# Kernel tuning notes

Measured on AMD Instinct MI355X. Metric: run time of the kernel, lower is better.

Reference implementation:

```python
import jax, jax.numpy as jnp
import numpy as np

NCONST = 100
NFEATS = 16
NCLASS = 5
NEFF = 6
NDYN = 6
BN_EPS = 1e-3  # keras BatchNormalization default epsilon


def _edge_indices(nconst):
    # itertools.product order, skipping self-pairs, matching _build_relation_matrices
    recv, send = [], []
    for i in range(nconst):
        for j in range(nconst):
            if i != j:
                recv.append(i)
                send.append(j)
    return np.asarray(recv, np.int32), np.asarray(send, np.int32)


def setup_inputs() -> dict:
    key = jax.random.key(0)
    ks = jax.random.split(key, 16)

    def w(k, shape, fan_in):
        return (jax.random.normal(k, shape, jnp.float32) / np.sqrt(fan_in)).astype(jnp.float32)

    inp = {
        "x": jax.random.normal(ks[0], (512, NCONST, NFEATS), jnp.float32),
        # batchnorm (inference-mode) params over the feature axis
        "bn_gamma": jnp.ones((NFEATS,), jnp.float32),
        "bn_beta": jnp.zeros((NFEATS,), jnp.float32),
        "bn_mean": jnp.zeros((NFEATS,), jnp.float32),
        "bn_var": jnp.ones((NFEATS,), jnp.float32),
        # fr: pointwise Conv1D == dense over last dim; 2*nfeats -> 30 -> 15 -> 6
        "fr_w1": w(ks[1], (2 * NFEATS, 30), 2 * NFEATS), "fr_b1": jnp.zeros((30,), jnp.float32),
        "fr_w2": w(ks[2], (30, 15), 30), "fr_b2": jnp.zeros((15,), jnp.float32),
        "fr_w3": w(ks[3], (15, NEFF), 15), "fr_b3": jnp.zeros((NEFF,), jnp.float32),
        # fo: (nfeats + neffects) -> 45 -> 22 -> 6
        "fo_w1": w(ks[4], (NFEATS + NEFF, 45), NFEATS + NEFF), "fo_b1": jnp.zeros((45,), jnp.float32),
        "fo_w2": w(ks[5], (45, 22), 45), "fo_b2": jnp.zeros((22,), jnp.float32),
        "fo_w3": w(ks[6], (22, NDYN), 22), "fo_b3": jnp.zeros((NDYN,), jnp.float32),
        # fc: ndyn -> 48 -> nclasses (softmax)
        "fc_w1": w(ks[7], (NDYN, 48), NDYN), "fc_b1": jnp.zeros((48,), jnp.float32),
        "fc_w2": w(ks[8], (48, NCLASS), 48), "fc_b2": jnp.zeros((NCLASS,), jnp.float32),
    }
    return inp


def reference(x, bn_gamma, bn_beta, bn_mean, bn_var,
              fr_w1, fr_b1, fr_w2, fr_b2, fr_w3, fr_b3,
              fo_w1, fo_b1, fo_w2, fo_b2, fo_w3, fo_b3,
              fc_w1, fc_b1, fc_w2, fc_b2):
    nconst = x.shape[1]
    recv_idx, send_idx = _edge_indices(nconst)  # static, shape (nedges,)

    # BatchNormalization (inference) over the feature axis: (B, N, F)
    xb = (x - bn_mean) * jax.lax.rsqrt(bn_var + BN_EPS) * bn_gamma + bn_beta

    # One-hot relation matmuls are exact gathers: (B, E, F) each.
    # Concat order matches Concatenate(axis=1)([receiver, sender]) pre-permute.
    fr_in = jnp.concatenate([xb[:, recv_idx, :], xb[:, send_idx, :]], axis=-1)  # (B, E, 2F)

    h = jax.nn.relu(fr_in @ fr_w1 + fr_b1)
    h = jax.nn.relu(h @ fr_w2 + fr_b2)
    effects = jax.nn.relu(h @ fr_w3 + fr_b3)  # (B, E, neff)

    # Multiplying by receiver_matrix^T is a scatter-add of edge effects to receiver nodes.
    agg = jnp.zeros((x.shape[0], nconst, effects.shape[-1]), effects.dtype)
    agg = agg.at[:, recv_idx, :].add(effects)  # (B, N, neff)

    fo_in = jnp.concatenate([xb, agg], axis=-1)  # (B, N, F + neff)
    d = jax.nn.relu(fo_in @ fo_w1 + fo_b1)
    d = jax.nn.relu(d @ fo_w2 + fo_b2)
    d = jax.nn.relu(d @ fo_w3 + fo_b3)  # (B, N, ndyn)

    fc_in = jnp.sum(d, axis=1)  # summation=True -> (B, ndyn)
    h = jax.nn.relu(fc_in @ fc_w1 + fc_b1)
    logits = h @ fc_w2 + fc_b2
    return jax.nn.softmax(logits, axis=-1)  # (B, nclasses)
```

## Files before the change

kernel.cpp:

```cpp
#include <hip/hip_runtime.h>
#include <math.h>

#define NCONST 100
#define NF     16
#define BLK    512

typedef _Float16 f16;
typedef _Float16 f16x8 __attribute__((ext_vector_type(8)));
typedef _Float16 f16x4 __attribute__((ext_vector_type(4)));
typedef float    f32x16 __attribute__((ext_vector_type(16)));

__global__ __launch_bounds__(BLK, 4) void convint_fused(
    const float* __restrict__ x,
    const float* __restrict__ bn_g, const float* __restrict__ bn_b,
    const float* __restrict__ bn_m, const float* __restrict__ bn_v,
    const float* __restrict__ frw1, const float* __restrict__ frb1,
    const float* __restrict__ frw2, const float* __restrict__ frb2,
    const float* __restrict__ frw3, const float* __restrict__ frb3,
    const float* __restrict__ fow1, const float* __restrict__ fob1,
    const float* __restrict__ fow2, const float* __restrict__ fob2,
    const float* __restrict__ fow3, const float* __restrict__ fob3,
    const float* __restrict__ fcw1, const float* __restrict__ fcb1,
    const float* __restrict__ fcw2, const float* __restrict__ fcb2,
    float* __restrict__ out)
{
    __shared__ float xbn[NCONST][NF];
    __shared__ float upool[7200];
    __shared__ float aggF[NCONST * 8];
    __shared__ float fcin[8];
    __shared__ float hfc[48];
    __shared__ float logits[8];

    char* const PrB = (char*)upool;
    char* const PsB = PrB + 8000;
    float (*const foh1)[48] = (float (*)[48])upool;
    float (*const foh2)[24] = (float (*)[24])(upool + 4800);

    const int b   = blockIdx.x;
    const int tid = threadIdx.x;
    const float* xb = x + (size_t)b * (NCONST * NF);

    for (int idx = tid; idx < NCONST * NF; idx += BLK) {
        int f = idx & 15;
        float sc = rsqrtf(bn_v[f] + 1e-3f) * bn_g[f];
        xbn[idx >> 4][f] = (xb[idx] - bn_m[f]) * sc + bn_b[f];
    }
    if (tid < 8) fcin[tid] = 0.f;
    __syncthreads();

    for (int idx = tid; idx < 1600; idx += BLK) {
        int n   = idx >> 4;
        int rem = idx & 15;
        int sel = rem >> 3;
        int oq  = rem & 7;
        int o0  = oq * 4;
        float xs[16];
        {
            const float4* xv = (const float4*)(&xbn[n][0]);
            float4 x0 = xv[0], x1 = xv[1], x2 = xv[2], x3 = xv[3];
            xs[0]=x0.x; xs[1]=x0.y; xs[2]=x0.z; xs[3]=x0.w;
            xs[4]=x1.x; xs[5]=x1.y; xs[6]=x1.z; xs[7]=x1.w;
            xs[8]=x2.x; xs[9]=x2.y; xs[10]=x2.z; xs[11]=x2.w;
            xs[12]=x3.x; xs[13]=x3.y; xs[14]=x3.z; xs[15]=x3.w;
        }
        float acc0 = (!sel) ? frb1[o0 + 0] : 0.f;
        float acc1 = (!sel) ? frb1[o0 + 1] : 0.f;
        float acc2 = (!sel && oq < 7) ? frb1[o0 + 2] : 0.f;
        float acc3 = (!sel && oq < 7) ? frb1[o0 + 3] : 0.f;
        const float* wbase = frw1 + sel * 16 * 30;
        const int wcol2 = (oq < 7) ? o0 + 2 : 28;
        #pragma unroll
        for (int f = 0; f < 16; ++f) {
            const float* wr = wbase + f * 30;
            float2 wa = *(const float2*)(wr + o0);
            float2 wb = *(const float2*)(wr + wcol2);
            acc0 = fmaf(xs[f], wa.x, acc0);
            acc1 = fmaf(xs[f], wa.y, acc1);
            acc2 = fmaf(xs[f], wb.x, acc2);
            acc3 = fmaf(xs[f], wb.y, acc3);
        }
        f16x4 hv;
        hv[0] = (f16)acc0;
        hv[1] = (f16)acc1;
        hv[2] = (oq < 7) ? (f16)acc2 : (sel ? (f16)0.f : (f16)1.f);
        hv[3] = (oq < 7) ? (f16)acc3 : (f16)0.f;
        int slot = oq >> 1;
        int sw = (slot & 2) | ((slot ^ (n >> 3)) & 1);
        *(f16x4*)((sel ? PsB : PrB) + n * 80 + sw * 16 + (oq & 1) * 8) = hv;
    }
    __syncthreads();

    {
        const int l  = tid & 63;
        const int wv = tid >> 6;
        const int e  = l & 31;
        const int hi = l >> 5;

        const int o2p = (e >= 4 && e < 12) ? (e ^ 12) : e;
        const bool o2v = (o2p < 15);
        const int  o2c = o2v ? o2p : 0;
        const bool o3v = (e < 6);
        const int  o3c = o3v ? e : 0;

        f16x8 bf1a, bf1b, bf2p;
        #pragma unroll
        for (int m = 0; m < 8; ++m) {
            int ka  = hi * 8 + m;
            int kb_ = 16 + ka;
            bf1a[m] = o2v ? (f16)frw2[ka * 15 + o2c] : (f16)0.f;
            f16 wb = (f16)0.f;
            if (o2v) {
                if (kb_ < 30)       wb = (f16)frw2[kb_ * 15 + o2c];
                else if (kb_ == 30) wb = (f16)frb2[o2c];
            }
            bf1b[m] = wb;
            f16 w3 = (f16)0.f;
            if (o3v) {
                if (ka < 15)       w3 = (f16)frw3[ka * 6 + o3c];
                else               w3 = (f16)frb3[o3c];
            }
            bf2p[m] = w3;
        }
        f32x16 cz;
        #pragma unroll
        for (int r = 0; r < 16; ++r) cz[r] = 0.f;
        const float gtail = (e < 3) ? 1.f : 0.f;

        for (int base = wv; base < 50; base += 8) {
            const int iA = base, iB = base + 50;
            const char* prpA = PrB + iA * 80 + ((hi ^ ((iA >> 3) & 1)) * 16);
            const char* prpB = PrB + iB * 80 + ((hi ^ ((iB >> 3) & 1)) * 16);
            f16x8 praA = *(const f16x8*)prpA;
            f16x8 prbA = *(const f16x8*)(prpA + 32);
            f16x8 praB = *(const f16x8*)prpB;
            f16x8 prbB = *(const f16x8*)(prpB + 32);
            float a0 = 0.f, a1 = 0.f, a2r = 0.f, a3 = 0.f;
            float b0 = 0.f, b1 = 0.f, b2r = 0.f, b3 = 0.f;

            int jA = iA + 1 + e; if (jA >= 100) jA -= 100;
            int jB = iB + 1 + e; if (jB >= 100) jB -= 100;
            #pragma unroll
            for (int tb = 0; tb < 4; ++tb) {
                const char* pspA = PsB + jA * 80 + ((hi ^ ((jA >> 3) & 1)) * 16);
                const char* pspB = PsB + jB * 80 + ((hi ^ ((jB >> 3) & 1)) * 16);
                f16x8 psaA = *(const f16x8*)pspA;
                f16x8 psbA = *(const f16x8*)(pspA + 32);
                f16x8 psaB = *(const f16x8*)pspB;
                f16x8 psbB = *(const f16x8*)(pspB + 32);

                f16x8 h1aA = praA + psaA, h1bA = prbA + psbA;
                f16x8 h1aB = praB + psaB, h1bB = prbB + psbB;
                #pragma unroll
                for (int m = 0; m < 8; ++m) {
                    h1aA[m] = (h1aA[m] > (f16)0.f) ? h1aA[m] : (f16)0.f;
                    h1bA[m] = (h1bA[m] > (f16)0.f) ? h1bA[m] : (f16)0.f;
                    h1aB[m] = (h1aB[m] > (f16)0.f) ? h1aB[m] : (f16)0.f;
                    h1bB[m] = (h1bB[m] > (f16)0.f) ? h1bB[m] : (f16)0.f;
                }
                f32x16 c1A = __builtin_amdgcn_mfma_f32_32x32x16_f16(bf1a, h1aA, cz, 0, 0, 0);
                f32x16 c1B = __builtin_amdgcn_mfma_f32_32x32x16_f16(bf1a, h1aB, cz, 0, 0, 0);
                c1A = __builtin_amdgcn_mfma_f32_32x32x16_f16(bf1b, h1bA, c1A, 0, 0, 0);
                c1B = __builtin_amdgcn_mfma_f32_32x32x16_f16(bf1b, h1bB, c1B, 0, 0, 0);

                union { int w[4]; f16x8 v; } aA, aB;
                aA.w[0] = __builtin_bit_cast(int, __builtin_amdgcn_cvt_pkrtz(c1A[0], c1A[1]));
                aA.w[1] = __builtin_bit_cast(int, __builtin_amdgcn_cvt_pkrtz(c1A[2], c1A[3]));
                aA.w[2] = __builtin_bit_cast(int, __builtin_amdgcn_cvt_pkrtz(c1A[4], c1A[5]));
                aA.w[3] = __builtin_bit_cast(int, __builtin_amdgcn_cvt_pkrtz(c1A[6], c1A[7]));
                aB.w[0] = __builtin_bit_cast(int, __builtin_amdgcn_cvt_pkrtz(c1B[0], c1B[1]));
                aB.w[1] = __builtin_bit_cast(int, __builtin_amdgcn_cvt_pkrtz(c1B[2], c1B[3]));
                aB.w[2] = __builtin_bit_cast(int, __builtin_amdgcn_cvt_pkrtz(c1B[4], c1B[5]));
                aB.w[3] = __builtin_bit_cast(int, __builtin_amdgcn_cvt_pkrtz(c1B[6], c1B[7]));
                #pragma unroll
                for (int m = 0; m < 8; ++m) {
                    aA.v[m] = (aA.v[m] > (f16)0.f) ? aA.v[m] : (f16)0.f;
                    aB.v[m] = (aB.v[m] > (f16)0.f) ? aB.v[m] : (f16)0.f;
                }
                aA.v[7] = hi ? (f16)1.f : aA.v[7];
                aB.v[7] = hi ? (f16)1.f : aB.v[7];

                f32x16 c2A = __builtin_amdgcn_mfma_f32_32x32x16_f16(bf2p, aA.v, cz, 0, 0, 0);
                f32x16 c2B = __builtin_amdgcn_mfma_f32_32x32x16_f16(bf2p, aB.v, cz, 0, 0, 0);

                if (tb < 3) {
                    a0 += fmaxf(c2A[0], 0.f);  a1 += fmaxf(c2A[1], 0.f);
                    a2r += fmaxf(c2A[2], 0.f); a3 += fmaxf(c2A[3], 0.f);
                    b0 += fmaxf(c2B[0], 0.f);  b1 += fmaxf(c2B[1], 0.f);
                    b2r += fmaxf(c2B[2], 0.f); b3 += fmaxf(c2B[3], 0.f);
                } else {
                    a0 = fmaf(gtail, fmaxf(c2A[0], 0.f), a0);
                    a1 = fmaf(gtail, fmaxf(c2A[1], 0.f), a1);
                    a2r = fmaf(gtail, fmaxf(c2A[2], 0.f), a2r);
                    a3 = fmaf(gtail, fmaxf(c2A[3], 0.f), a3);
                    b0 = fmaf(gtail, fmaxf(c2B[0], 0.f), b0);
                    b1 = fmaf(gtail, fmaxf(c2B[1], 0.f), b1);
                    b2r = fmaf(gtail, fmaxf(c2B[2], 0.f), b2r);
                    b3 = fmaf(gtail, fmaxf(c2B[3], 0.f), b3);
                }
                jA += 32; if (jA >= 100) jA -= 100;
                jB += 32; if (jB >= 100) jB -= 100;
            }
            #pragma unroll
            for (int mk = 1; mk <= 16; mk <<= 1) {
                a0 += __shfl_xor(a0, mk);  a1 += __shfl_xor(a1, mk);
                a2r += __shfl_xor(a2r, mk); a3 += __shfl_xor(a3, mk);
                b0 += __shfl_xor(b0, mk);  b1 += __shfl_xor(b1, mk);
                b2r += __shfl_xor(b2r, mk); b3 += __shfl_xor(b3, mk);
            }
            if (l == 0) {
                float4 v; v.x = a0; v.y = a1; v.z = a2r; v.w = a3;
                *(float4*)&aggF[iA * 8] = v;
                float4 w; w.x = b0; w.y = b1; w.z = b2r; w.w = b3;
                *(float4*)&aggF[iB * 8] = w;
            } else if (l == 32) {
                float2 v; v.x = a0; v.y = a1;
                *(float2*)&aggF[iA * 8 + 4] = v;
                float2 w; w.x = b0; w.y = b1;
                *(float2*)&aggF[iB * 8 + 4] = w;
            }
        }
    }
    __syncthreads();

    for (int idx = tid; idx < NCONST * 45; idx += BLK) {
        int n = idx / 45, o = idx - n * 45;
        float acc = fob1[o];
        const float4* xv = (const float4*)(&xbn[n][0]);
        #pragma unroll
        for (int q = 0; q < 4; ++q) {
            float4 xq = xv[q];
            acc = fmaf(xq.x, fow1[(4 * q + 0) * 45 + o], acc);
            acc = fmaf(xq.y, fow1[(4 * q + 1) * 45 + o], acc);
            acc = fmaf(xq.z, fow1[(4 * q + 2) * 45 + o], acc);
            acc = fmaf(xq.w, fow1[(4 * q + 3) * 45 + o], acc);
        }
        const float4 g0 = *(const float4*)(&aggF[n * 8]);
        const float2 g1 = *(const float2*)(&aggF[n * 8 + 4]);
        acc = fmaf(g0.x, fow1[16 * 45 + o], acc);
        acc = fmaf(g0.y, fow1[17 * 45 + o], acc);
        acc = fmaf(g0.z, fow1[18 * 45 + o], acc);
        acc = fmaf(g0.w, fow1[19 * 45 + o], acc);
        acc = fmaf(g1.x, fow1[20 * 45 + o], acc);
        acc = fmaf(g1.y, fow1[21 * 45 + o], acc);
        foh1[n][o] = fmaxf(acc, 0.f);
    }
    __syncthreads();
    for (int idx = tid; idx < NCONST * 22; idx += BLK) {
        int n = idx / 22, o = idx - n * 22;
        float acc = fob2[o];
        const float4* hv = (const float4*)(&foh1[n][0]);
        #pragma unroll
        for (int q = 0; q < 11; ++q) {
            float4 h4 = hv[q];
            acc = fmaf(h4.x, fow2[(4 * q + 0) * 22 + o], acc);
            acc = fmaf(h4.y, fow2[(4 * q + 1) * 22 + o], acc);
            acc = fmaf(h4.z, fow2[(4 * q + 2) * 22 + o], acc);
            acc = fmaf(h4.w, fow2[(4 * q + 3) * 22 + o], acc);
        }
        acc = fmaf(foh1[n][44], fow2[44 * 22 + o], acc);
        foh2[n][o] = fmaxf(acc, 0.f);
    }
    __syncthreads();
    for (int idx = tid; idx < NCONST * 6; idx += BLK) {
        int n = idx / 6, c = idx - n * 6;
        float acc = fob3[c];
        const float4* hv = (const float4*)(&foh2[n][0]);
        #pragma unroll
        for (int q = 0; q < 5; ++q) {
            float4 h4 = hv[q];
            acc = fmaf(h4.x, fow3[(4 * q + 0) * 6 + c], acc);
            acc = fmaf(h4.y, fow3[(4 * q + 1) * 6 + c], acc);
            acc = fmaf(h4.z, fow3[(4 * q + 2) * 6 + c], acc);
            acc = fmaf(h4.w, fow3[(4 * q + 3) * 6 + c], acc);
        }
        acc = fmaf(foh2[n][20], fow3[20 * 6 + c], acc);
        acc = fmaf(foh2[n][21], fow3[21 * 6 + c], acc);
        atomicAdd(&fcin[c], fmaxf(acc, 0.f));
    }
    __syncthreads();
    if (tid < 48) {
        float acc = fcb1[tid];
        #pragma unroll
        for (int k = 0; k < 6; ++k) acc = fmaf(fcin[k], fcw1[k * 48 + tid], acc);
        hfc[tid] = fmaxf(acc, 0.f);
    }
    __syncthreads();
    if (tid < 5) {
        float acc = fcb2[tid];
        #pragma unroll
        for (int k = 0; k < 48; ++k) acc = fmaf(hfc[k], fcw2[k * 5 + tid], acc);
        logits[tid] = acc;
    }
    __syncthreads();
    if (tid == 0) {
        float m = logits[0];
        #pragma unroll
        for (int c = 1; c < 5; ++c) m = fmaxf(m, logits[c]);
        float ex[5], sum = 0.f;
        #pragma unroll
        for (int c = 0; c < 5; ++c) { ex[c] = __expf(logits[c] - m); sum += ex[c]; }
        float inv = 1.f / sum;
        #pragma unroll
        for (int c = 0; c < 5; ++c) out[(size_t)b * 5 + c] = ex[c] * inv;
    }
}

extern "C" void kernel_launch(void* const* d_in, const int* in_sizes, int n_in,
                              void* d_out, int out_size, void* d_ws, size_t ws_size,
                              hipStream_t stream) {
    const float* x     = (const float*)d_in[0];
    const float* bn_g  = (const float*)d_in[1];
    const float* bn_b  = (const float*)d_in[2];
    const float* bn_m  = (const float*)d_in[3];
    const float* bn_v  = (const float*)d_in[4];
    const float* frw1  = (const float*)d_in[5];
    const float* frb1  = (const float*)d_in[6];
    const float* frw2  = (const float*)d_in[7];
    const float* frb2  = (const float*)d_in[8];
    const float* frw3  = (const float*)d_in[9];
    const float* frb3  = (const float*)d_in[10];
    const float* fow1  = (const float*)d_in[11];
    const float* fob1  = (const float*)d_in[12];
    const float* fow2  = (const float*)d_in[13];
    const float* fob2  = (const float*)d_in[14];
    const float* fow3  = (const float*)d_in[15];
    const float* fob3  = (const float*)d_in[16];
    const float* fcw1  = (const float*)d_in[17];
    const float* fcb1  = (const float*)d_in[18];
    const float* fcw2  = (const float*)d_in[19];
    const float* fcb2  = (const float*)d_in[20];

    const int B = in_sizes[0] / (NCONST * NF);

    convint_fused<<<dim3(B), dim3(BLK), 0, stream>>>(
        x, bn_g, bn_b, bn_m, bn_v,
        frw1, frb1, frw2, frb2, frw3, frb3,
        fow1, fob1, fow2, fob2, fow3, fob3,
        fcw1, fcb1, fcw2, fcb2,
        (float*)d_out);
}
```

Baseline: 60.65 us.

## Fuse fo MLP layers per node in registers, dropping shared-memory staging

Replaces the three separate fo layers, each with its own shared-memory staging and block barrier, with one per-node pass that keeps the 45- and 22-wide hidden activations in registers. Only 100 threads (25 lanes in each of 4 waves) do the work, reading uniform weight addresses. This also shrinks the shared pool, which may allow more blocks per CU. The cost is far less parallelism in this phase and high register pressure, so the serial per-thread chain of roughly 2000 FMAs could end up slower than the spread-out version.

```diff
diff --git a/kernel.cpp b/kernel.cpp
--- a/kernel.cpp
+++ b/kernel.cpp
@@ -25,7 +25,7 @@
     float* __restrict__ out)
 {
     __shared__ float xbn[NCONST][NF];
-    __shared__ float upool[7200];
+    __shared__ float upool[4000];
     __shared__ float aggF[NCONST * 8];
     __shared__ float fcin[8];
     __shared__ float hfc[48];
@@ -33,8 +33,6 @@
 
     char* const PrB = (char*)upool;
     char* const PsB = PrB + 8000;
-    float (*const foh1)[48] = (float (*)[48])upool;
-    float (*const foh2)[24] = (float (*)[24])(upool + 4800);
 
     const int b   = blockIdx.x;
     const int tid = threadIdx.x;
@@ -222,62 +220,59 @@
     }
     __syncthreads();
 
-    for (int idx = tid; idx < NCONST * 45; idx += BLK) {
-        int n = idx / 45, o = idx - n * 45;
-        float acc = fob1[o];
-        const float4* xv = (const float4*)(&xbn[n][0]);
-        #pragma unroll
-        for (int q = 0; q < 4; ++q) {
-            float4 xq = xv[q];
-            acc = fmaf(xq.x, fow1[(4 * q + 0) * 45 + o], acc);
-            acc = fmaf(xq.y, fow1[(4 * q + 1) * 45 + o], acc);
-            acc = fmaf(xq.z, fow1[(4 * q + 2) * 45 + o], acc);
-            acc = fmaf(xq.w, fow1[(4 * q + 3) * 45 + o], acc);
-        }
-        const float4 g0 = *(const float4*)(&aggF[n * 8]);
-        const float2 g1 = *(const float2*)(&aggF[n * 8 + 4]);
-        acc = fmaf(g0.x, fow1[16 * 45 + o], acc);
-        acc = fmaf(g0.y, fow1[17 * 45 + o], acc);
-        acc = fmaf(g0.z, fow1[18 * 45 + o], acc);
-        acc = fmaf(g0.w, fow1[19 * 45 + o], acc);
-        acc = fmaf(g1.x, fow1[20 * 45 + o], acc);
-        acc = fmaf(g1.y, fow1[21 * 45 + o], acc);
-        foh1[n][o] = fmaxf(acc, 0.f);
-    }
-    __syncthreads();
-    for (int idx = tid; idx < NCONST * 22; idx += BLK) {
-        int n = idx / 22, o = idx - n * 22;
-        float acc = fob2[o];
-        const float4* hv = (const float4*)(&foh1[n][0]);
-        #pragma unroll
-        for (int q = 0; q < 11; ++q) {
-            float4 h4 = hv[q];
-            acc = fmaf(h4.x, fow2[(4 * q + 0) * 22 + o], acc);
-            acc = fmaf(h4.y, fow2[(4 * q + 1) * 22 + o], acc);
-            acc = fmaf(h4.z, fow2[(4 * q + 2) * 22 + o], acc);
-            acc = fmaf(h4.w, fow2[(4 * q + 3) * 22 + o], acc);
-        }
-        acc = fmaf(foh1[n][44], fow2[44 * 22 + o], acc);
-        foh2[n][o] = fmaxf(acc, 0.f);
-    }
-    __syncthreads();
-    for (int idx = tid; idx < NCONST * 6; idx += BLK) {
-        int n = idx / 6, c = idx - n * 6;
-        float acc = fob3[c];
-        const float4* hv = (const float4*)(&foh2[n][0]);
-        #pragma unroll
-        for (int q = 0; q < 5; ++q) {
-            float4 h4 = hv[q];
-            acc = fmaf(h4.x, fow3[(4 * q + 0) * 6 + c], acc);
-            acc = fmaf(h4.y, fow3[(4 * q + 1) * 6 + c], acc);
-            acc = fmaf(h4.z, fow3[(4 * q + 2) * 6 + c], acc);
-            acc = fmaf(h4.w, fow3[(4 * q + 3) * 6 + c], acc);
-        }
-        acc = fmaf(foh2[n][20], fow3[20 * 6 + c], acc);
-        acc = fmaf(foh2[n][21], fow3[21 * 6 + c], acc);
-        atomicAdd(&fcin[c], fmaxf(acc, 0.f));
-    }
-    __syncthreads();
+    {
+        const int wvF = tid >> 6;
+        const int lF  = tid & 63;
+        if (wvF < 4 && lF < 25) {
+            const int n = wvF * 25 + lF;
+            float in[22];
+            {
+                const float4* xv = (const float4*)(&xbn[n][0]);
+                float4 q0 = xv[0], q1 = xv[1], q2 = xv[2], q3 = xv[3];
+                in[0]=q0.x;  in[1]=q0.y;  in[2]=q0.z;  in[3]=q0.w;
+                in[4]=q1.x;  in[5]=q1.y;  in[6]=q1.z;  in[7]=q1.w;
+                in[8]=q2.x;  in[9]=q2.y;  in[10]=q2.z; in[11]=q2.w;
+                in[12]=q3.x; in[13]=q3.y; in[14]=q3.z; in[15]=q3.w;
+                const float4 g0 = *(const float4*)(&aggF[n * 8]);
+                const float2 g1 = *(const float2*)(&aggF[n * 8 + 4]);
+                in[16]=g0.x; in[17]=g0.y; in[18]=g0.z; in[19]=g0.w;
+                in[20]=g1.x; in[21]=g1.y;
+            }
+            float h1[45];
+            #pragma unroll
+            for (int o = 0; o < 45; ++o) h1[o] = fob1[o];
+            #pragma unroll
+            for (int k = 0; k < 22; ++k) {
+                float v = in[k];
+                #pragma unroll
+                for (int o = 0; o < 45; ++o) h1[o] = fmaf(v, fow1[k * 45 + o], h1[o]);
+            }
+            #pragma unroll
+            for (int o = 0; o < 45; ++o) h1[o] = fmaxf(h1[o], 0.f);
+
+            float h2[22];
+            #pragma unroll
+            for (int o = 0; o < 22; ++o) h2[o] = fob2[o];
+            #pragma unroll
+            for (int k = 0; k < 45; ++k) {
+                float v = h1[k];
+                #pragma unroll
+                for (int o = 0; o < 22; ++o) h2[o] = fmaf(v, fow2[k * 22 + o], h2[o]);
+            }
+            #pragma unroll
+            for (int o = 0; o < 22; ++o) h2[o] = fmaxf(h2[o], 0.f);
+
+            #pragma unroll
+            for (int c = 0; c < 6; ++c) {
+                float acc = fob3[c];
+                #pragma unroll
+                for (int k = 0; k < 22; ++k) acc = fmaf(h2[k], fow3[k * 6 + c], acc);
+                atomicAdd(&fcin[c], fmaxf(acc, 0.f));
+            }
+        }
+    }
+    __syncthreads();
+
     if (tid < 48) {
         float acc = fcb1[tid];
         #pragma unroll
```

Result: no change. 61.08 us, median of 2 (+0.7%).
